# Kernel tuning notes

Hardware: AMD Instinct MI355X
Metric: run time of the kernel (lower is better)

The kernel has to match this reference:

```python
import jax, jax.numpy as jnp
import numpy as np
from jax import lax

KERNEL = 15
IGNORE = 255


def setup_inputs() -> dict:
    key = jax.random.key(0)
    k1, k2 = jax.random.split(key)
    B, C, H, W = 32, 2, 480, 864
    logits = jax.random.normal(k1, (B, C, H, W), dtype=jnp.float32)
    labels = jax.random.randint(k2, (B, H, W), 0, 2, dtype=jnp.int32)
    return {"logits": logits, "labels": labels}


def _boundary_edgemap(labels):
    # labels: [B, H, W] int32 with values in {0, 1, IGNORE}
    lbl = labels.astype(jnp.int32)
    # np_label = label*255, with ignore pixels set to 0 (matches cv2 path)
    np_label = jnp.where(lbl == IGNORE, 0, lbl * 255)
    win = (1, KERNEL, KERNEL)
    strides = (1, 1, 1)
    # cv2.erode with ones kernel == 15x15 min filter (border value +inf -> pad 255)
    erosion = lax.reduce_window(np_label, jnp.int32(255), lax.min, win, strides, "SAME")
    # cv2.dilate == 15x15 max filter (border value -inf -> pad 0)
    dilation = lax.reduce_window(np_label, jnp.int32(0), lax.max, win, strides, "SAME")
    boundary = dilation - erosion  # >0 exactly on the morphological boundary band
    edgemap = jnp.where(boundary > 0, lbl, IGNORE)
    edgemap = jnp.where(lbl == IGNORE, IGNORE, edgemap)
    return edgemap


def reference(logits, labels):
    # logits: [B, C, H, W] log-probabilities, labels: [B, H, W]
    edgemap = _boundary_edgemap(labels)  # [B, H, W]
    valid = edgemap != IGNORE
    tgt = jnp.where(valid, edgemap, 0)  # safe index for ignored pixels
    # gather logits[b, tgt, h, w] -> [B, H, W]
    picked = jnp.take_along_axis(logits, tgt[:, None, :, :], axis=1)[:, 0]
    # NLLLoss with ignore_index: mean of -logp over valid pixels
    n_valid = jnp.maximum(jnp.sum(valid), 1)
    loss = -jnp.sum(jnp.where(valid, picked, 0.0)) / n_valid.astype(logits.dtype)
    return loss
```

## Files before the change

kernel.cpp:

```cpp
#include <hip/hip_runtime.h>


namespace {
constexpr int B_ = 32;
constexpr int H_ = 480;
constexpr int W_ = 864;
constexpr int HW = H_ * W_;
constexpr int R_ = 7;
constexpr int TH_ = 16;
constexpr int LH = TH_ + 2 * R_;
constexpr int SW = 216;
constexpr int NSX = W_ / SW;
constexpr int NSY = H_ / TH_;
constexpr int NBLK = B_ * NSX * NSY;
}

typedef unsigned long long u64;

__device__ __forceinline__ u64 shfl_up64(u64 x, int d) {
  return __shfl_up(x, d, 64);
}
__device__ __forceinline__ u64 shfl_dn64(u64 x, int d) {
  return __shfl_down(x, d, 64);
}

extern "C" __global__ __launch_bounds__(64, 4)
void boundary_loss_main(const float* __restrict__ logits,
                        const int* __restrict__ labels,
                        double2* __restrict__ partials)
{
  const int lane = threadIdx.x;
  const int bid = blockIdx.x;
  const int lb = (bid & 7) * (NBLK / 8) + (bid >> 3);
  const int img = lb / (NSX * NSY);
  const int r = lb - img * (NSX * NSY);
  const int strip = r / NSY;
  const int seg = r - strip * NSY;
  const int gr0 = seg * TH_;

  const int cb0 = strip * SW - 8 + 4 * lane;
  const bool colinb = (cb0 >= 0) && (cb0 + 3 < W_);
  const int cbc = colinb ? cb0 : (cb0 < 0 ? 0 : W_ - 4);
  const bool labok = colinb && (lane < 58);
  const bool outl = (lane >= 2) && (lane < 56);

  const int* __restrict__ lab = labels + img * HW + cbc;
  const float* __restrict__ lg = logits + (size_t)(2 * img) * HW;
  const float* pg = lg + (size_t)gr0 * W_ + cb0;

  u64 f0 = 0, f1 = 0, f2 = 0, f3 = 0;
  unsigned cp0 = 0, cp1 = 0, cp2 = 0, cp3 = 0;
#pragma unroll
  for (int a = 0; a < LH; ++a) {
    int gr = gr0 - R_ + a;
    gr = gr < 0 ? 0 : (gr >= H_ ? H_ - 1 : gr);
    const int4 v = *(const int4*)(lab + gr * W_);
    const unsigned e1x = (v.x == 1), e1y = (v.y == 1),
                   e1z = (v.z == 1), e1w = (v.w == 1);
    f0 |= (u64)(1u + e1x) << (2 * a);
    f1 |= (u64)(1u + e1y) << (2 * a);
    f2 |= (u64)(1u + e1z) << (2 * a);
    f3 |= (u64)(1u + e1w) << (2 * a);
    if (a >= R_ && a < R_ + TH_) {
      const int sh = 2 * (a - R_);
      cp0 |= (e1x | ((unsigned)(v.x == 255) << 1)) << sh;
      cp1 |= (e1y | ((unsigned)(v.y == 255) << 1)) << sh;
      cp2 |= (e1z | ((unsigned)(v.z == 255) << 1)) << sh;
      cp3 |= (e1w | ((unsigned)(v.w == 255) << 1)) << sh;
    }
  }
  {
    const int tv = gr0 == 0 ? R_ : 0;
    const int hi = LH < (H_ + R_ - gr0) ? LH : (H_ + R_ - gr0);
    u64 rm = (hi - tv >= 32) ? ((((1ull << (2 * (hi - tv) - 32)) - 1ull) << 32)
                                | 0xFFFFFFFFull)
                             : ((1ull << (2 * (hi - tv))) - 1ull);
    rm <<= 2 * tv;
    if (!colinb) rm = 0;
    f0 &= rm; f1 &= rm; f2 &= rm; f3 &= rm;
  }

  float4 a0[8], a1[8];
  if (outl) {
#pragma unroll
    for (int o = 0; o < 8; ++o) {
      a0[o] = *(const float4*)(pg + (size_t)o * W_);
      a1[o] = *(const float4*)(pg + (size_t)o * W_ + HW);
    }
  }

  const u64 allf = f0 | f1 | f2 | f3;
  const u64 s2 = f2 | f3, s3 = f1 | s2;
  const u64 p2 = f0 | f1, p3 = p2 | f2;
  const u64 core = shfl_up64(allf, 1) | allf | shfl_dn64(allf, 1);
  u64 w0 = core | shfl_up64(s3, 2);
  u64 w1 = core | shfl_up64(s2, 2) | shfl_dn64(f0, 2);
  u64 w2 = core | shfl_up64(f3, 2) | shfl_dn64(p2, 2);
  u64 w3 = core | shfl_dn64(p3, 2);

  w0 |= w0 >> 2;  w0 |= w0 >> 4;  w0 |= w0 >> 8;  w0 |= w0 >> 14;
  w1 |= w1 >> 2;  w1 |= w1 >> 4;  w1 |= w1 >> 8;  w1 |= w1 >> 14;
  w2 |= w2 >> 2;  w2 |= w2 >> 4;  w2 |= w2 >> 8;  w2 |= w2 >> 14;
  w3 |= w3 >> 2;  w3 |= w3 >> 4;  w3 |= w3 >> 8;  w3 |= w3 >> 14;

  double lsum = 0.0;
  unsigned lcnt = 0;

  if (outl) {
#pragma unroll
    for (int o = 0; o < 8; ++o) {
      const unsigned b0 = (unsigned)(w0 >> (2 * o)) & 3u;
      const unsigned b1 = (unsigned)(w1 >> (2 * o)) & 3u;
      const unsigned b2 = (unsigned)(w2 >> (2 * o)) & 3u;
      const unsigned b3 = (unsigned)(w3 >> (2 * o)) & 3u;
      const unsigned q0 = (cp0 >> (2 * o)) & 3u;
      const unsigned q1 = (cp1 >> (2 * o)) & 3u;
      const unsigned q2 = (cp2 >> (2 * o)) & 3u;
      const unsigned q3 = (cp3 >> (2 * o)) & 3u;
      const float4 a = a0[o], c = a1[o];
      const bool k0 = (b0 == 3u) && !(q0 & 2u);
      const bool k1 = (b1 == 3u) && !(q1 & 2u);
      const bool k2 = (b2 == 3u) && !(q2 & 2u);
      const bool k3 = (b3 == 3u) && !(q3 & 2u);
      lsum += k0 ? (double)((q0 & 1u) ? c.x : a.x) : 0.0;
      lsum += k1 ? (double)((q1 & 1u) ? c.y : a.y) : 0.0;
      lsum += k2 ? (double)((q2 & 1u) ? c.z : a.z) : 0.0;
      lsum += k3 ? (double)((q3 & 1u) ? c.w : a.w) : 0.0;
      lcnt += (unsigned)k0 + k1 + k2 + k3;
    }
  }
  float4 b0v[8], b1v[8];
  if (outl) {
    const float* p_ = pg + (size_t)8 * W_;
#pragma unroll
    for (int o = 0; o < 8; ++o) {
      b0v[o] = *(const float4*)(p_ + (size_t)o * W_);
      b1v[o] = *(const float4*)(p_ + (size_t)o * W_ + HW);
    }
#pragma unroll
    for (int o = 0; o < 8; ++o) {
      const int ro = 8 + o;
      const unsigned b0 = (unsigned)(w0 >> (2 * ro)) & 3u;
      const unsigned b1 = (unsigned)(w1 >> (2 * ro)) & 3u;
      const unsigned b2 = (unsigned)(w2 >> (2 * ro)) & 3u;
      const unsigned b3 = (unsigned)(w3 >> (2 * ro)) & 3u;
      const unsigned q0 = (cp0 >> (2 * ro)) & 3u;
      const unsigned q1 = (cp1 >> (2 * ro)) & 3u;
      const unsigned q2 = (cp2 >> (2 * ro)) & 3u;
      const unsigned q3 = (cp3 >> (2 * ro)) & 3u;
      const float4 a = b0v[o], c = b1v[o];
      const bool k0 = (b0 == 3u) && !(q0 & 2u);
      const bool k1 = (b1 == 3u) && !(q1 & 2u);
      const bool k2 = (b2 == 3u) && !(q2 & 2u);
      const bool k3 = (b3 == 3u) && !(q3 & 2u);
      lsum += k0 ? (double)((q0 & 1u) ? c.x : a.x) : 0.0;
      lsum += k1 ? (double)((q1 & 1u) ? c.y : a.y) : 0.0;
      lsum += k2 ? (double)((q2 & 1u) ? c.z : a.z) : 0.0;
      lsum += k3 ? (double)((q3 & 1u) ? c.w : a.w) : 0.0;
      lcnt += (unsigned)k0 + k1 + k2 + k3;
    }
  }

#pragma unroll
  for (int off = 32; off > 0; off >>= 1) {
    lsum += __shfl_down(lsum, off, 64);
    lcnt += __shfl_down(lcnt, off, 64);
  }
  if (lane == 0) partials[bid] = make_double2(lsum, (double)lcnt);
}

extern "C" __global__ __launch_bounds__(1024)
void boundary_loss_final(const double2* __restrict__ partials,
                         float* __restrict__ out)
{
  __shared__ double red_s[16];
  __shared__ double red_c[16];
  const int tid = threadIdx.x;
  double s = 0.0, c = 0.0;
  for (int i = tid; i < NBLK; i += 1024) {
    const double2 p = partials[i];
    s += p.x;
    c += p.y;
  }
#pragma unroll
  for (int off = 32; off > 0; off >>= 1) {
    s += __shfl_down(s, off, 64);
    c += __shfl_down(c, off, 64);
  }
  const int wave = tid >> 6;
  if ((tid & 63) == 0) { red_s[wave] = s; red_c[wave] = c; }
  __syncthreads();
  if (tid == 0) {
    double ts = 0.0, tc = 0.0;
#pragma unroll
    for (int i = 0; i < 16; ++i) { ts += red_s[i]; tc += red_c[i]; }
    if (tc < 1.0) tc = 1.0;
    out[0] = (float)(-ts / tc);
  }
}

extern "C" void kernel_launch(void* const* d_in, const int* in_sizes, int n_in,
                              void* d_out, int out_size, void* d_ws, size_t ws_size,
                              hipStream_t stream)
{
  const float* logits = (const float*)d_in[0];
  const int* labels = (const int*)d_in[1];
  float* out = (float*)d_out;
  double2* partials = (double2*)d_ws;

  boundary_loss_main<<<dim3(NBLK), 64, 0, stream>>>(logits, labels, partials);
  boundary_loss_final<<<1, 1024, 0, stream>>>(partials, out);
}
```

Measured before the change: 219.5 us.

## Double-buffer logits loads in 4-row groups with sched barriers

```diff
diff --git a/kernel.cpp b/kernel.cpp
--- a/kernel.cpp
+++ b/kernel.cpp
@@ -24,7 +24,7 @@
   return __shfl_down(x, d, 64);
 }
 
-extern "C" __global__ __launch_bounds__(64, 4)
+extern "C" __global__ __launch_bounds__(64, 2)
 void boundary_loss_main(const float* __restrict__ logits,
                         const int* __restrict__ labels,
                         double2* __restrict__ partials)
@@ -72,22 +72,25 @@
   {
     const int tv = gr0 == 0 ? R_ : 0;
     const int hi = LH < (H_ + R_ - gr0) ? LH : (H_ + R_ - gr0);
-    u64 rm = (hi - tv >= 32) ? ((((1ull << (2 * (hi - tv) - 32)) - 1ull) << 32)
-                                | 0xFFFFFFFFull)
-                             : ((1ull << (2 * (hi - tv))) - 1ull);
+    u64 rm = (2 * (hi - tv) >= 32)
+                 ? ((((1ull << (2 * (hi - tv) - 32)) - 1ull) << 32) | 0xFFFFFFFFull)
+                 : ((1ull << (2 * (hi - tv))) - 1ull);
     rm <<= 2 * tv;
     if (!colinb) rm = 0;
     f0 &= rm; f1 &= rm; f2 &= rm; f3 &= rm;
   }
 
-  float4 a0[8], a1[8];
-  if (outl) {
-#pragma unroll
-    for (int o = 0; o < 8; ++o) {
-      a0[o] = *(const float4*)(pg + (size_t)o * W_);
-      a1[o] = *(const float4*)(pg + (size_t)o * W_ + HW);
-    }
+  float4 qa0[4], qa1[4], qb0[4], qb1[4];
+#define ISSUE(G0, G1, q)                                                    \
+  if (outl) {                                                               \
+    const float* p_ = pg + (size_t)(4 * (q)) * W_;                          \
+    _Pragma("unroll") for (int o = 0; o < 4; ++o) {                         \
+      G0[o] = *(const float4*)(p_ + (size_t)o * W_);                        \
+      G1[o] = *(const float4*)(p_ + (size_t)o * W_ + HW);                   \
+    }                                                                       \
   }
+
+  ISSUE(qa0, qa1, 0)
 
   const u64 allf = f0 | f1 | f2 | f3;
   const u64 s2 = f2 | f3, s3 = f1 | s2;
@@ -105,61 +108,43 @@
 
   double lsum = 0.0;
   unsigned lcnt = 0;
+#define CONSUME(G0, G1, q)                                                  \
+  if (outl) {                                                               \
+    _Pragma("unroll") for (int o = 0; o < 4; ++o) {                         \
+      const int ro = 4 * (q) + o;                                           \
+      const unsigned b0 = (unsigned)(w0 >> (2 * ro)) & 3u;                  \
+      const unsigned b1 = (unsigned)(w1 >> (2 * ro)) & 3u;                  \
+      const unsigned b2 = (unsigned)(w2 >> (2 * ro)) & 3u;                  \
+      const unsigned b3 = (unsigned)(w3 >> (2 * ro)) & 3u;                  \
+      const unsigned q0 = (cp0 >> (2 * ro)) & 3u;                           \
+      const unsigned q1 = (cp1 >> (2 * ro)) & 3u;                           \
+      const unsigned q2 = (cp2 >> (2 * ro)) & 3u;                           \
+      const unsigned q3 = (cp3 >> (2 * ro)) & 3u;                           \
+      const float4 a = G0[o], c = G1[o];                                    \
+      const bool k0 = (b0 == 3u) && !(q0 & 2u);                             \
+      const bool k1 = (b1 == 3u) && !(q1 & 2u);                             \
+      const bool k2 = (b2 == 3u) && !(q2 & 2u);                             \
+      const bool k3 = (b3 == 3u) && !(q3 & 2u);                             \
+      lsum += k0 ? (double)((q0 & 1u) ? c.x : a.x) : 0.0;                   \
+      lsum += k1 ? (double)((q1 & 1u) ? c.y : a.y) : 0.0;                   \
+      lsum += k2 ? (double)((q2 & 1u) ? c.z : a.z) : 0.0;                   \
+      lsum += k3 ? (double)((q3 & 1u) ? c.w : a.w) : 0.0;                   \
+      lcnt += (unsigned)k0 + k1 + k2 + k3;                                  \
+    }                                                                       \
+  }
 
-  if (outl) {
-#pragma unroll
-    for (int o = 0; o < 8; ++o) {
-      const unsigned b0 = (unsigned)(w0 >> (2 * o)) & 3u;
-      const unsigned b1 = (unsigned)(w1 >> (2 * o)) & 3u;
-      const unsigned b2 = (unsigned)(w2 >> (2 * o)) & 3u;
-      const unsigned b3 = (unsigned)(w3 >> (2 * o)) & 3u;
-      const unsigned q0 = (cp0 >> (2 * o)) & 3u;
-      const unsigned q1 = (cp1 >> (2 * o)) & 3u;
-      const unsigned q2 = (cp2 >> (2 * o)) & 3u;
-      const unsigned q3 = (cp3 >> (2 * o)) & 3u;
-      const float4 a = a0[o], c = a1[o];
-      const bool k0 = (b0 == 3u) && !(q0 & 2u);
-      const bool k1 = (b1 == 3u) && !(q1 & 2u);
-      const bool k2 = (b2 == 3u) && !(q2 & 2u);
-      const bool k3 = (b3 == 3u) && !(q3 & 2u);
-      lsum += k0 ? (double)((q0 & 1u) ? c.x : a.x) : 0.0;
-      lsum += k1 ? (double)((q1 & 1u) ? c.y : a.y) : 0.0;
-      lsum += k2 ? (double)((q2 & 1u) ? c.z : a.z) : 0.0;
-      lsum += k3 ? (double)((q3 & 1u) ? c.w : a.w) : 0.0;
-      lcnt += (unsigned)k0 + k1 + k2 + k3;
-    }
-  }
-  float4 b0v[8], b1v[8];
-  if (outl) {
-    const float* p_ = pg + (size_t)8 * W_;
-#pragma unroll
-    for (int o = 0; o < 8; ++o) {
-      b0v[o] = *(const float4*)(p_ + (size_t)o * W_);
-      b1v[o] = *(const float4*)(p_ + (size_t)o * W_ + HW);
-    }
-#pragma unroll
-    for (int o = 0; o < 8; ++o) {
-      const int ro = 8 + o;
-      const unsigned b0 = (unsigned)(w0 >> (2 * ro)) & 3u;
-      const unsigned b1 = (unsigned)(w1 >> (2 * ro)) & 3u;
-      const unsigned b2 = (unsigned)(w2 >> (2 * ro)) & 3u;
-      const unsigned b3 = (unsigned)(w3 >> (2 * ro)) & 3u;
-      const unsigned q0 = (cp0 >> (2 * ro)) & 3u;
-      const unsigned q1 = (cp1 >> (2 * ro)) & 3u;
-      const unsigned q2 = (cp2 >> (2 * ro)) & 3u;
-      const unsigned q3 = (cp3 >> (2 * ro)) & 3u;
-      const float4 a = b0v[o], c = b1v[o];
-      const bool k0 = (b0 == 3u) && !(q0 & 2u);
-      const bool k1 = (b1 == 3u) && !(q1 & 2u);
-      const bool k2 = (b2 == 3u) && !(q2 & 2u);
-      const bool k3 = (b3 == 3u) && !(q3 & 2u);
-      lsum += k0 ? (double)((q0 & 1u) ? c.x : a.x) : 0.0;
-      lsum += k1 ? (double)((q1 & 1u) ? c.y : a.y) : 0.0;
-      lsum += k2 ? (double)((q2 & 1u) ? c.z : a.z) : 0.0;
-      lsum += k3 ? (double)((q3 & 1u) ? c.w : a.w) : 0.0;
-      lcnt += (unsigned)k0 + k1 + k2 + k3;
-    }
-  }
+  ISSUE(qb0, qb1, 1)
+  CONSUME(qa0, qa1, 0)
+  __builtin_amdgcn_sched_barrier(0);
+  ISSUE(qa0, qa1, 2)
+  CONSUME(qb0, qb1, 1)
+  __builtin_amdgcn_sched_barrier(0);
+  ISSUE(qb0, qb1, 3)
+  CONSUME(qa0, qa1, 2)
+  __builtin_amdgcn_sched_barrier(0);
+  CONSUME(qb0, qb1, 3)
+#undef ISSUE
+#undef CONSUME
 
 #pragma unroll
   for (int off = 32; off > 0; off >>= 1) {
```

New measurement: 194.5 us, median of 2. -11.4%, faster.
